# Kernel optimization log

Hardware: AMD Instinct MI355X
Metric: run time of the kernel (lower is better)

The kernel has to match this reference:

```python
import jax, jax.numpy as jnp
import numpy as np

B, C, H, W = 8, 256, 128, 128
CQ = C // 8


def setup_inputs() -> dict:
    key = jax.random.key(0)
    ks = jax.random.split(key, 8)
    s = 1.0 / np.sqrt(C)
    return {
        "x": jax.random.normal(ks[0], (B, C, H, W), dtype=jnp.float32),
        "wq": jax.random.normal(ks[1], (CQ, C), dtype=jnp.float32) * s,
        "bq": jax.random.normal(ks[2], (CQ,), dtype=jnp.float32) * 0.01,
        "wk": jax.random.normal(ks[3], (CQ, C), dtype=jnp.float32) * s,
        "bk": jax.random.normal(ks[4], (CQ,), dtype=jnp.float32) * 0.01,
        "wv": jax.random.normal(ks[5], (C, C), dtype=jnp.float32) * s,
        "bv": jax.random.normal(ks[6], (C,), dtype=jnp.float32) * 0.01,
        "gamma": jax.random.normal(ks[7], (1,), dtype=jnp.float32) * 0.1,
    }


def reference(x, wq, bq, wk, bk, wv, bv, gamma):
    b, c, h, w = x.shape
    # 1x1 convs == channel matmuls
    q = jnp.einsum("oc,bchw->bohw", wq, x) + bq[None, :, None, None]  # [B,Cq,H,W]
    k = jnp.einsum("oc,bchw->bohw", wk, x) + bk[None, :, None, None]  # [B,Cq,H,W]
    v = jnp.einsum("oc,bchw->bohw", wv, x) + bv[None, :, None, None]  # [B,C,H,W]

    # column (height) scores: energy_H[b,i,w,j] = <k[:, i, w], q[:, j, w]>, -inf on i==j
    e_h = jnp.einsum("bciw,bcjw->biwj", k, q)  # [B,H,W,H]
    diag = jnp.eye(h, dtype=bool)[:, None, :]  # [H,1,H] -> masks i==j
    e_h = jnp.where(diag[None], -jnp.inf, e_h)

    # row (width) scores: energy_W[b,h,i,j] = <k[:, h, i], q[:, h, j]>
    e_w = jnp.einsum("bchi,bchj->bhij", k, q)  # [B,H,W,W]

    # joint softmax over concatenated H+W scores (axis 3), as in the torch code
    att = jax.nn.softmax(jnp.concatenate([e_h, e_w], axis=3), axis=3)
    a_h, a_w = att[..., :h], att[..., h:]

    out_h = jnp.einsum("bciw,biwj->bcjw", v, a_h)  # aggregate along column
    out_w = jnp.einsum("bchi,bhij->bchj", v, a_w)  # aggregate along row
    return gamma * (out_h + out_w) + x
```

## Files before the change

### kernel.cpp

```cpp
#include <hip/hip_runtime.h>
#include <math.h>

#define C_   256
#define CQ_  32
#define H_   128
#define W_   128
#define HW_  (H_ * W_)
#define OC_  320

typedef __attribute__((ext_vector_type(8))) short  s8v;
typedef __attribute__((ext_vector_type(4))) float  f4v;
typedef __attribute__((ext_vector_type(8))) unsigned short u8v;
typedef __attribute__((ext_vector_type(4))) unsigned short u4v;

__device__ inline unsigned short f2bf(float f) {
    unsigned int u = __float_as_uint(f);
    unsigned int r = (u + 0x7fffu + ((u >> 16) & 1u)) >> 16;
    return (unsigned short)r;
}
__device__ inline float bfu(unsigned short u) {
    return __uint_as_float((unsigned int)u << 16);
}

__global__ __launch_bounds__(256) void k_wconv(
    const float* __restrict__ wq, const float* __restrict__ wk,
    const float* __restrict__ wv, unsigned short* __restrict__ Wb)
{
    int idx4 = blockIdx.x * 256 + threadIdx.x;
    int e = idx4 * 4;
    int oc = e >> 8, k = e & 255;
    const float* src;
    if (oc < 32)      src = wq + (size_t)oc * C_ + k;
    else if (oc < 64) src = wk + (size_t)(oc - 32) * C_ + k;
    else              src = wv + (size_t)(oc - 64) * C_ + k;
    float4 v = *(const float4*)src;
    u4v o;
    o[0] = f2bf(v.x); o[1] = f2bf(v.y); o[2] = f2bf(v.z); o[3] = f2bf(v.w);
    *(u4v*)(Wb + e) = o;
}

__global__ __launch_bounds__(256) void k_qkv(
    const float* __restrict__ x, const unsigned short* __restrict__ Wb,
    const float* __restrict__ bq, const float* __restrict__ bk,
    const float* __restrict__ bv,
    unsigned short* __restrict__ qkv, int b0)
{
    __shared__ __align__(16) unsigned short Wl[2][64][72];
    __shared__ __align__(16) unsigned int   Xp[2][32 * 132];
    const int t = threadIdx.x;
    const int lane = t & 63;
    const int wave = t >> 6;
    const int n0 = blockIdx.x * 128;
    const int ocblk = blockIdx.y * 64;
    const int bb = blockIdx.z;
    const float* xb = x + (size_t)(b0 + bb) * C_ * HW_;

    const int lg = lane >> 4;
    const int ll = lane & 15;
    const int n_w = wave * 32;

    const int kp8 = t >> 5;
    const int n4  = (t & 31) * 4;
    const int wrow = t >> 3;
    const int wcg  = (t & 7) * 8;
    float4 ra[4], rb[4];
    u8v wreg[2];

    #pragma unroll
    for (int p = 0; p < 4; ++p) {
        int krow = (p * 8 + kp8) * 2;
        ra[p] = *(const float4*)(xb + (size_t)krow * HW_ + n0 + n4);
        rb[p] = *(const float4*)(xb + (size_t)(krow + 1) * HW_ + n0 + n4);
    }
    #pragma unroll
    for (int q = 0; q < 2; ++q)
        wreg[q] = *(const u8v*)(Wb + (size_t)(ocblk + wrow + q * 32) * C_ + wcg);

    #pragma unroll
    for (int p = 0; p < 4; ++p) {
        uint4 d;
        const float* af  = (const float*)&ra[p];
        const float* bf_ = (const float*)&rb[p];
        #pragma unroll
        for (int i = 0; i < 4; ++i) {
            unsigned int lo = (__float_as_uint(af[i])  + 0x8000u) >> 16;
            unsigned int hi = (__float_as_uint(bf_[i]) + 0x8000u) & 0xffff0000u;
            ((unsigned int*)&d)[i] = hi | lo;
        }
        *(uint4*)&Xp[0][(p * 8 + kp8) * 132 + n4] = d;
    }
    #pragma unroll
    for (int q = 0; q < 2; ++q)
        *(u8v*)&Wl[0][wrow + q * 32][wcg] = wreg[q];

    #pragma unroll
    for (int p = 0; p < 4; ++p) {
        int krow = 64 + (p * 8 + kp8) * 2;
        ra[p] = *(const float4*)(xb + (size_t)krow * HW_ + n0 + n4);
        rb[p] = *(const float4*)(xb + (size_t)(krow + 1) * HW_ + n0 + n4);
    }
    #pragma unroll
    for (int q = 0; q < 2; ++q)
        wreg[q] = *(const u8v*)(Wb + (size_t)(ocblk + wrow + q * 32) * C_ + 64 + wcg);

    f4v acc[4][2];
    #pragma unroll
    for (int mr = 0; mr < 4; ++mr)
        #pragma unroll
        for (int nr = 0; nr < 2; ++nr)
            acc[mr][nr] = (f4v){0.f, 0.f, 0.f, 0.f};

    __syncthreads();

    #pragma unroll
    for (int kc = 0; kc < 4; ++kc) {
        const int cur = kc & 1;
        if (kc < 3) {
            #pragma unroll
            for (int p = 0; p < 4; ++p) {
                uint4 d;
                const float* af  = (const float*)&ra[p];
                const float* bf_ = (const float*)&rb[p];
                #pragma unroll
                for (int i = 0; i < 4; ++i) {
                    unsigned int lo = (__float_as_uint(af[i])  + 0x8000u) >> 16;
                    unsigned int hi = (__float_as_uint(bf_[i]) + 0x8000u) & 0xffff0000u;
                    ((unsigned int*)&d)[i] = hi | lo;
                }
                *(uint4*)&Xp[cur ^ 1][(p * 8 + kp8) * 132 + n4] = d;
            }
            #pragma unroll
            for (int q = 0; q < 2; ++q)
                *(u8v*)&Wl[cur ^ 1][wrow + q * 32][wcg] = wreg[q];
        }
        if (kc < 2) {
            #pragma unroll
            for (int p = 0; p < 4; ++p) {
                int krow = (kc + 2) * 64 + (p * 8 + kp8) * 2;
                ra[p] = *(const float4*)(xb + (size_t)krow * HW_ + n0 + n4);
                rb[p] = *(const float4*)(xb + (size_t)(krow + 1) * HW_ + n0 + n4);
            }
            #pragma unroll
            for (int q = 0; q < 2; ++q)
                wreg[q] = *(const u8v*)(
                    Wb + (size_t)(ocblk + wrow + q * 32) * C_ + (kc + 2) * 64 + wcg);
        }
        #pragma unroll
        for (int ks = 0; ks < 2; ++ks) {
            s8v afr[4];
            #pragma unroll
            for (int mr = 0; mr < 4; ++mr)
                afr[mr] = *(const s8v*)&Wl[cur][mr * 16 + ll][ks * 32 + lg * 8];
            #pragma unroll
            for (int nr = 0; nr < 2; ++nr) {
                int4 bd;
                #pragma unroll
                for (int e2 = 0; e2 < 4; ++e2)
                    ((int*)&bd)[e2] =
                        Xp[cur][(ks * 16 + lg * 4 + e2) * 132 + n_w + nr * 16 + ll];
                s8v bfr = *(s8v*)&bd;
                #pragma unroll
                for (int mr = 0; mr < 4; ++mr)
                    acc[mr][nr] = __builtin_amdgcn_mfma_f32_16x16x32_bf16(
                        afr[mr], bfr, acc[mr][nr], 0, 0, 0);
            }
        }
        __syncthreads();
    }

    #pragma unroll
    for (int mr = 0; mr < 4; ++mr) {
        float bias[4];
        #pragma unroll
        for (int r = 0; r < 4; ++r) {
            int oc = ocblk + mr * 16 + lg * 4 + r;
            if (oc < 32)      bias[r] = bq[oc];
            else if (oc < 64) bias[r] = bk[oc - 32];
            else              bias[r] = bv[oc - 64];
        }
        #pragma unroll
        for (int nr = 0; nr < 2; ++nr) {
            int n = n0 + n_w + nr * 16 + ll;
            #pragma unroll
            for (int r = 0; r < 4; ++r) {
                int oc = ocblk + mr * 16 + lg * 4 + r;
                qkv[((size_t)bb * OC_ + oc) * HW_ + n] = f2bf(acc[mr][nr][r] + bias[r]);
            }
        }
    }
}

__global__ __launch_bounds__(256) void k_transpose_qkv(
    const unsigned short* __restrict__ qkv, unsigned short* __restrict__ qkv_t)
{
    __shared__ unsigned short tile[32][34];
    const int bb = blockIdx.z;
    const int oc = blockIdx.y;
    const int th = (blockIdx.x & 3) * 32;
    const int tw = (blockIdx.x >> 2) * 32;
    const unsigned short* src = qkv + ((size_t)bb * OC_ + oc) * HW_;
    #pragma unroll
    for (int r = 0; r < 4; ++r) {
        int h = threadIdx.y * 4 + r;
        tile[h][threadIdx.x] = src[(size_t)(th + h) * W_ + tw + threadIdx.x];
    }
    __syncthreads();
    unsigned short* dst = qkv_t + (size_t)bb * W_ * OC_ * H_;
    #pragma unroll
    for (int r = 0; r < 4; ++r) {
        int wl = threadIdx.y * 4 + r;
        dst[((size_t)(tw + wl) * OC_ + oc) * H_ + th + threadIdx.x] = tile[threadIdx.x][wl];
    }
}

__device__ inline void stage_KQ(const unsigned short* base, int cstride,
                                unsigned int* Ktp, unsigned int* Qp, int t)
{
    {
        int i = t & 127, half = t >> 7, c0 = half * 16;
        unsigned int kr[16];
        #pragma unroll
        for (int cc = 0; cc < 16; ++cc)
            kr[cc] = base[(size_t)(32 + c0 + cc) * cstride + i];
        uint4 d0, d1;
        #pragma unroll
        for (int e2 = 0; e2 < 4; ++e2)
            ((unsigned int*)&d0)[e2] = kr[2 * e2] | (kr[2 * e2 + 1] << 16);
        #pragma unroll
        for (int e2 = 0; e2 < 4; ++e2)
            ((unsigned int*)&d1)[e2] = kr[8 + 2 * e2] | (kr[9 + 2 * e2] << 16);
        *(uint4*)&Ktp[i * 20 + half * 8]     = d0;
        *(uint4*)&Ktp[i * 20 + half * 8 + 4] = d1;
    }
    {
        int c2 = t >> 4, j8 = (t & 15) * 8;
        u8v qa = *(const u8v*)(base + (size_t)(2 * c2) * cstride + j8);
        u8v qb = *(const u8v*)(base + (size_t)(2 * c2 + 1) * cstride + j8);
        uint4 e0, e1;
        #pragma unroll
        for (int e = 0; e < 4; ++e)
            ((unsigned int*)&e0)[e] =
                (unsigned int)qa[e] | ((unsigned int)qb[e] << 16);
        #pragma unroll
        for (int e = 0; e < 4; ++e)
            ((unsigned int*)&e1)[e] =
                (unsigned int)qa[4 + e] | ((unsigned int)qb[4 + e] << 16);
        *(uint4*)&Qp[c2 * 132 + j8]     = e0;
        *(uint4*)&Qp[c2 * 132 + j8 + 4] = e1;
    }
}

__device__ inline f4v eqk_mfma(const unsigned int* Ktp, const unsigned int* Qp,
                               int mr, int j, int lg, int ll)
{
    s8v afr = *(const s8v*)&Ktp[(mr * 16 + ll) * 20 + lg * 4];
    int4 bd;
    #pragma unroll
    for (int e2 = 0; e2 < 4; ++e2)
        ((int*)&bd)[e2] = Qp[(lg * 4 + e2) * 132 + j];
    s8v bfr = *(s8v*)&bd;
    return __builtin_amdgcn_mfma_f32_16x16x32_bf16(
        afr, bfr, (f4v){0.f, 0.f, 0.f, 0.f}, 0, 0, 0);
}

__global__ __launch_bounds__(256) void k_stats_h(
    const unsigned short* __restrict__ qkv_t,
    float* __restrict__ mh, float* __restrict__ sh)
{
    __shared__ __align__(16) unsigned int Ktp[128 * 20];
    __shared__ __align__(16) unsigned int Qp[16 * 132];
    const int t = threadIdx.x;
    const int beta = blockIdx.x;
    const int bb = blockIdx.y;
    const unsigned short* base = qkv_t + ((size_t)bb * W_ + beta) * OC_ * H_;
    stage_KQ(base, H_, Ktp, Qp, t);
    __syncthreads();

    const int lane = t & 63;
    const int wv = t >> 6;
    const int lg = lane >> 4;
    const int ll = lane & 15;

    #pragma unroll
    for (int ml = 0; ml < 2; ++ml) {
        const int mr = wv * 2 + ml;
        const int i0 = mr * 16 + lg * 4;
        f4v ef[8];
        #pragma unroll
        for (int nt = 0; nt < 8; ++nt) {
            f4v e = eqk_mfma(Ktp, Qp, mr, nt * 16 + ll, lg, ll);
            int j = nt * 16 + ll;
            #pragma unroll
            for (int r = 0; r < 4; ++r)
                if (i0 + r == j) e[r] = -INFINITY;
            ef[nt] = e;
        }
        #pragma unroll
        for (int r = 0; r < 4; ++r) {
            float mm = -INFINITY;
            #pragma unroll
            for (int nt = 0; nt < 8; ++nt) mm = fmaxf(mm, ef[nt][r]);
            #pragma unroll
            for (int s = 1; s < 16; s <<= 1) mm = fmaxf(mm, __shfl_xor(mm, s));
            float ss = 0.f;
            #pragma unroll
            for (int nt = 0; nt < 8; ++nt) ss += __expf(ef[nt][r] - mm);
            #pragma unroll
            for (int s = 1; s < 16; s <<= 1) ss += __shfl_xor(ss, s);
            if (ll == 0) {
                int i = i0 + r;
                mh[((size_t)bb * H_ + i) * W_ + beta] = mm;
                sh[((size_t)bb * H_ + i) * W_ + beta] = ss;
            }
        }
    }
}

__global__ __launch_bounds__(256) void k_stats_w(
    const unsigned short* __restrict__ qkv,
    float* __restrict__ mw, float* __restrict__ sw)
{
    __shared__ __align__(16) unsigned int Ktp[128 * 20];
    __shared__ __align__(16) unsigned int Qp[16 * 132];
    const int t = threadIdx.x;
    const int alpha = blockIdx.x;
    const int bb = blockIdx.y;
    const unsigned short* base = qkv + (size_t)bb * OC_ * HW_ + (size_t)alpha * W_;
    stage_KQ(base, HW_, Ktp, Qp, t);
    __syncthreads();

    const int lane = t & 63;
    const int wv = t >> 6;
    const int lg = lane >> 4;
    const int ll = lane & 15;

    #pragma unroll
    for (int ml = 0; ml < 2; ++ml) {
        const int mr = wv * 2 + ml;
        const int i0 = mr * 16 + lg * 4;
        f4v ef[8];
        #pragma unroll
        for (int nt = 0; nt < 8; ++nt)
            ef[nt] = eqk_mfma(Ktp, Qp, mr, nt * 16 + ll, lg, ll);
        #pragma unroll
        for (int r = 0; r < 4; ++r) {
            float mm = -INFINITY;
            #pragma unroll
            for (int nt = 0; nt < 8; ++nt) mm = fmaxf(mm, ef[nt][r]);
            #pragma unroll
            for (int s = 1; s < 16; s <<= 1) mm = fmaxf(mm, __shfl_xor(mm, s));
            float ss = 0.f;
            #pragma unroll
            for (int nt = 0; nt < 8; ++nt) ss += __expf(ef[nt][r] - mm);
            #pragma unroll
            for (int s = 1; s < 16; s <<= 1) ss += __shfl_xor(ss, s);
            if (ll == 0) {
                int i = i0 + r;
                mw[((size_t)bb * H_ + alpha) * W_ + i] = mm;
                sw[((size_t)bb * H_ + alpha) * W_ + i] = ss;
            }
        }
    }
}

__global__ __launch_bounds__(256) void k_prep(
    const float* __restrict__ mh, const float* __restrict__ sh,
    const float* __restrict__ mw, const float* __restrict__ sw,
    float* __restrict__ mc, float* __restrict__ dv,
    float* __restrict__ mct, float* __restrict__ dvt, int n)
{
    int idx = blockIdx.x * 256 + threadIdx.x;
    if (idx >= n) return;
    float m1 = mh[idx], s1 = sh[idx], m2 = mw[idx], s2 = sw[idx];
    float m = fmaxf(m1, m2);
    float d = 1.f / (s1 * __expf(m1 - m) + s2 * __expf(m2 - m));
    mc[idx] = m; dv[idx] = d;
    int q = idx & (W_ - 1);
    int p = (idx >> 7) & (H_ - 1);
    int b = idx >> 14;
    size_t tid = ((size_t)b * W_ + q) * H_ + p;
    mct[tid] = m; dvt[tid] = d;
}

__global__ __launch_bounds__(256) void k_outh(
    const unsigned short* __restrict__ qkv_t,
    const float* __restrict__ mct, const float* __restrict__ dvt,
    unsigned short* __restrict__ oh_t)
{
    __shared__ __align__(16) unsigned short Pt[128 * 128];
    __shared__ __align__(16) unsigned char  Ubuf[18688];
    __shared__ float mloc[128], dloc[128];
    unsigned int* Ktp = (unsigned int*)Ubuf;
    unsigned int* Qp  = (unsigned int*)(Ubuf + 10240);
    unsigned short* Vl = (unsigned short*)Ubuf;

    const int t = threadIdx.x;
    const int beta = blockIdx.x;
    const int bb = blockIdx.y;
    const unsigned short* base = qkv_t + ((size_t)bb * W_ + beta) * OC_ * H_;

    if (t < 128) {
        size_t sidx = ((size_t)bb * W_ + beta) * H_ + t;
        mloc[t] = mct[sidx];
        dloc[t] = dvt[sidx];
    }
    stage_KQ(base, H_, Ktp, Qp, t);

    const int vc  = t >> 4;
    const int vi0 = (t & 15) * 8;
    u8v vreg[4];
    {
        const unsigned short* vsrc = base + (size_t)64 * H_;
        #pragma unroll
        for (int q = 0; q < 4; ++q)
            vreg[q] = *(const u8v*)(vsrc + (size_t)(vc + q * 16) * H_ + vi0);
    }
    __syncthreads();

    const int lane = t & 63;
    const int wv = t >> 6;
    const int lg = lane >> 4;
    const int ll = lane & 15;
    const int jq0 = wv * 32;

    #pragma unroll
    for (int mr = 0; mr < 8; ++mr) {
        const int i0 = mr * 16 + lg * 4;
        float mi[4], di[4];
        #pragma unroll
        for (int r = 0; r < 4; ++r) { mi[r] = mloc[i0 + r]; di[r] = dloc[i0 + r]; }
        #pragma unroll
        for (int nt = 0; nt < 2; ++nt) {
            int j = jq0 + nt * 16 + ll;
            f4v e = eqk_mfma(Ktp, Qp, mr, j, lg, ll);
            float p0 = (i0     == j) ? 0.f : __expf(e[0] - mi[0]) * di[0];
            float p1 = (i0 + 1 == j) ? 0.f : __expf(e[1] - mi[1]) * di[1];
            float p2 = (i0 + 2 == j) ? 0.f : __expf(e[2] - mi[2]) * di[2];
            float p3 = (i0 + 3 == j) ? 0.f : __expf(e[3] - mi[3]) * di[3];
            uint2 wd;
            wd.x = f2bf(p0) | ((unsigned int)f2bf(p1) << 16);
            wd.y = f2bf(p2) | ((unsigned int)f2bf(p3) << 16);
            int sidx = (j * 128 + i0) ^ ((j & 7) << 3);
            *(uint2*)&Pt[sidx] = wd;
        }
    }

    unsigned short* outbase = oh_t + ((size_t)bb * W_ + beta) * C_ * H_;
    const int cw = (wv & 1) * 32;
    const int jw = (wv >> 1) * 64;

    for (int ch = 0; ch < 4; ++ch) {
        __syncthreads();
        #pragma unroll
        for (int q = 0; q < 4; ++q) {
            int c = vc + q * 16;
            *(u8v*)&Vl[(c * 128 + vi0) ^ ((c & 7) << 3)] = vreg[q];
        }
        __syncthreads();
        if (ch < 3) {
            const unsigned short* vsrc = base + (size_t)(64 + (ch + 1) * 64) * H_;
            #pragma unroll
            for (int q = 0; q < 4; ++q)
                vreg[q] = *(const u8v*)(vsrc + (size_t)(vc + q * 16) * H_ + vi0);
        }

        f4v acc[2][4];
        #pragma unroll
        for (int cr = 0; cr < 2; ++cr)
            #pragma unroll
            for (int nt = 0; nt < 4; ++nt)
                acc[cr][nt] = (f4v){0.f, 0.f, 0.f, 0.f};

        #pragma unroll
        for (int kk = 0; kk < 4; ++kk) {
            s8v afr[2];
            #pragma unroll
            for (int cr = 0; cr < 2; ++cr) {
                int crow = cw + cr * 16 + ll;
                afr[cr] = *(const s8v*)&Vl[(crow * 128 + kk * 32 + lg * 8) ^ ((crow & 7) << 3)];
            }
            #pragma unroll
            for (int nt = 0; nt < 4; ++nt) {
                int j = jw + nt * 16 + ll;
                s8v bfr = *(const s8v*)&Pt[(j * 128 + kk * 32 + lg * 8) ^ ((j & 7) << 3)];
                acc[0][nt] = __builtin_amdgcn_mfma_f32_16x16x32_bf16(afr[0], bfr, acc[0][nt], 0, 0, 0);
                acc[1][nt] = __builtin_amdgcn_mfma_f32_16x16x32_bf16(afr[1], bfr, acc[1][nt], 0, 0, 0);
            }
        }
        #pragma unroll
        for (int cr = 0; cr < 2; ++cr)
            #pragma unroll
            for (int nt = 0; nt < 4; ++nt) {
                int j = jw + nt * 16 + ll;
                #pragma unroll
                for (int r = 0; r < 4; ++r) {
                    int c = ch * 64 + cw + cr * 16 + lg * 4 + r;
                    outbase[(size_t)c * H_ + j] = f2bf(acc[cr][nt][r]);
                }
            }
    }
}

__global__ __launch_bounds__(256) void k_outw(
    const unsigned short* __restrict__ qkv,
    const float* __restrict__ mc, const float* __restrict__ dv_,
    unsigned short* __restrict__ ow)
{
    __shared__ __align__(16) unsigned short Pt[128 * 128];
    __shared__ __align__(16) unsigned char  Ubuf[18688];
    __shared__ float mloc[128], dloc[128];
    unsigned int* Ktp = (unsigned int*)Ubuf;
    unsigned int* Qp  = (unsigned int*)(Ubuf + 10240);
    unsigned short* Vl = (unsigned short*)Ubuf;

    const int t = threadIdx.x;
    const int alpha = blockIdx.x;
    const int bb = blockIdx.y;
    const unsigned short* base = qkv + (size_t)bb * OC_ * HW_ + (size_t)alpha * W_;

    if (t < 128) {
        size_t sidx = ((size_t)bb * H_ + alpha) * W_ + t;
        mloc[t] = mc[sidx];
        dloc[t] = dv_[sidx];
    }
    stage_KQ(base, HW_, Ktp, Qp, t);

    const int vc  = t >> 4;
    const int vi0 = (t & 15) * 8;
    u8v vreg[4];
    {
        const unsigned short* vsrc = base + (size_t)64 * HW_;
        #pragma unroll
        for (int q = 0; q < 4; ++q)
            vreg[q] = *(const u8v*)(vsrc + (size_t)(vc + q * 16) * HW_ + vi0);
    }
    __syncthreads();

    const int lane = t & 63;
    const int wv = t >> 6;
    const int lg = lane >> 4;
    const int ll = lane & 15;
    const int jq0 = wv * 32;

    #pragma unroll
    for (int mr = 0; mr < 8; ++mr) {
        const int i0 = mr * 16 + lg * 4;
        float mi[4], di[4];
        #pragma unroll
        for (int r = 0; r < 4; ++r) { mi[r] = mloc[i0 + r]; di[r] = dloc[i0 + r]; }
        #pragma unroll
        for (int nt = 0; nt < 2; ++nt) {
            int j = jq0 + nt * 16 + ll;
            f4v e = eqk_mfma(Ktp, Qp, mr, j, lg, ll);
            float p0 = __expf(e[0] - mi[0]) * di[0];
            float p1 = __expf(e[1] - mi[1]) * di[1];
            float p2 = __expf(e[2] - mi[2]) * di[2];
            float p3 = __expf(e[3] - mi[3]) * di[3];
            uint2 wd;
            wd.x = f2bf(p0) | ((unsigned int)f2bf(p1) << 16);
            wd.y = f2bf(p2) | ((unsigned int)f2bf(p3) << 16);
            int sidx = (j * 128 + i0) ^ ((j & 7) << 3);
            *(uint2*)&Pt[sidx] = wd;
        }
    }

    unsigned short* obase = ow + (size_t)bb * C_ * HW_ + (size_t)alpha * W_;
    const int cw = (wv & 1) * 32;
    const int jw = (wv >> 1) * 64;

    for (int ch = 0; ch < 4; ++ch) {
        __syncthreads();
        #pragma unroll
        for (int q = 0; q < 4; ++q) {
            int c = vc + q * 16;
            *(u8v*)&Vl[(c * 128 + vi0) ^ ((c & 7) << 3)] = vreg[q];
        }
        __syncthreads();
        if (ch < 3) {
            const unsigned short* vsrc = base + (size_t)(64 + (ch + 1) * 64) * HW_;
            #pragma unroll
            for (int q = 0; q < 4; ++q)
                vreg[q] = *(const u8v*)(vsrc + (size_t)(vc + q * 16) * HW_ + vi0);
        }

        f4v acc[2][4];
        #pragma unroll
        for (int cr = 0; cr < 2; ++cr)
            #pragma unroll
            for (int nt = 0; nt < 4; ++nt)
                acc[cr][nt] = (f4v){0.f, 0.f, 0.f, 0.f};

        #pragma unroll
        for (int kk = 0; kk < 4; ++kk) {
            s8v afr[2];
            #pragma unroll
            for (int cr = 0; cr < 2; ++cr) {
                int crow = cw + cr * 16 + ll;
                afr[cr] = *(const s8v*)&Vl[(crow * 128 + kk * 32 + lg * 8) ^ ((crow & 7) << 3)];
            }
            #pragma unroll
            for (int nt = 0; nt < 4; ++nt) {
                int j = jw + nt * 16 + ll;
                s8v bfr = *(const s8v*)&Pt[(j * 128 + kk * 32 + lg * 8) ^ ((j & 7) << 3)];
                acc[0][nt] = __builtin_amdgcn_mfma_f32_16x16x32_bf16(afr[0], bfr, acc[0][nt], 0, 0, 0);
                acc[1][nt] = __builtin_amdgcn_mfma_f32_16x16x32_bf16(afr[1], bfr, acc[1][nt], 0, 0, 0);
            }
        }
        #pragma unroll
        for (int cr = 0; cr < 2; ++cr)
            #pragma unroll
            for (int nt = 0; nt < 4; ++nt) {
                int j = jw + nt * 16 + ll;
                #pragma unroll
                for (int r = 0; r < 4; ++r) {
                    int c = ch * 64 + cw + cr * 16 + lg * 4 + r;
                    obase[(size_t)c * HW_ + j] = f2bf(acc[cr][nt][r]);
                }
            }
    }
}

__global__ __launch_bounds__(256) void k_combine(
    const unsigned short* __restrict__ oh_t, const unsigned short* __restrict__ ow,
    const float* __restrict__ x, const float* __restrict__ gamma_p,
    float* __restrict__ out, int b0)
{
    __shared__ unsigned short tile[128][130];
    const int t  = threadIdx.x;
    const int c  = blockIdx.x;
    const int bb = blockIdx.y;
    const float gamma = gamma_p[0];

    {
        const unsigned short* src = oh_t + (size_t)bb * W_ * C_ * H_ + (size_t)c * H_;
        const int row = t >> 1;
        const int h0  = (t & 1) * 64;
        #pragma unroll
        for (int q = 0; q < 8; ++q) {
            u8v v = *(const u8v*)(src + (size_t)row * (C_ * H_) + h0 + q * 8);
            *(u8v*)&tile[row][h0 + q * 8] = v;
        }
    }
    __syncthreads();

    const size_t pbase = ((size_t)bb * C_ + c) * HW_;
    const size_t gbase = ((size_t)(b0 + bb) * C_ + c) * HW_;
    const int w4 = (t & 31) * 4;
    const int hb = t >> 5;
    #pragma unroll
    for (int hh = 0; hh < 16; ++hh) {
        int h = hb + hh * 8;
        size_t idx = (size_t)h * W_ + w4;
        float4 xv = *(const float4*)(x + gbase + idx);
        u4v o4 = *(const u4v*)(ow + pbase + idx);
        float4 r;
        r.x = xv.x + gamma * (bfu(o4[0]) + bfu(tile[w4 + 0][h]));
        r.y = xv.y + gamma * (bfu(o4[1]) + bfu(tile[w4 + 1][h]));
        r.z = xv.z + gamma * (bfu(o4[2]) + bfu(tile[w4 + 2][h]));
        r.w = xv.w + gamma * (bfu(o4[3]) + bfu(tile[w4 + 3][h]));
        *(float4*)(out + gbase + idx) = r;
    }
}

extern "C" void kernel_launch(void* const* d_in, const int* in_sizes, int n_in,
                              void* d_out, int out_size, void* d_ws, size_t ws_size,
                              hipStream_t stream)
{
    (void)in_sizes; (void)n_in; (void)out_size;
    const float* x  = (const float*)d_in[0];
    const float* wq = (const float*)d_in[1];
    const float* bq = (const float*)d_in[2];
    const float* wk = (const float*)d_in[3];
    const float* bk = (const float*)d_in[4];
    const float* wv = (const float*)d_in[5];
    const float* bv = (const float*)d_in[6];
    const float* gm = (const float*)d_in[7];
    float* out = (float*)d_out;

    const size_t e_qkv  = (size_t)OC_ * HW_;
    const size_t e_out  = (size_t)C_ * HW_;
    const size_t e_stat = (size_t)HW_;
    const size_t perb_bytes = (e_qkv * 2 + e_out * 2) * 2 + e_stat * 8 * 4;
    const size_t wb_bytes = (size_t)OC_ * C_ * 2;
    int nbcap = (int)((ws_size - wb_bytes) / perb_bytes);
    if (nbcap > 8) nbcap = 8;
    if (nbcap < 1) nbcap = 1;

    unsigned short* Wb    = (unsigned short*)d_ws;
    unsigned short* qkv   = Wb    + (size_t)OC_ * C_;
    unsigned short* qkv_t = qkv   + e_qkv * nbcap;
    unsigned short* oh    = qkv_t + e_qkv * nbcap;
    unsigned short* ow    = oh    + e_out * nbcap;
    float* mh  = (float*)(ow + e_out * nbcap);
    float* sh  = mh  + e_stat * nbcap;
    float* mw  = sh  + e_stat * nbcap;
    float* sw  = mw  + e_stat * nbcap;
    float* mc  = sw  + e_stat * nbcap;
    float* dv  = mc  + e_stat * nbcap;
    float* mct = dv  + e_stat * nbcap;
    float* dvt = mct + e_stat * nbcap;

    k_wconv<<<dim3(80), 256, 0, stream>>>(wq, wk, wv, Wb);

    for (int b0 = 0; b0 < 8; b0 += nbcap) {
        int nb = 8 - b0 < nbcap ? 8 - b0 : nbcap;
        k_qkv<<<dim3(HW_ / 128, 5, nb), 256, 0, stream>>>(
            x, Wb, bq, bk, bv, qkv, b0);
        k_transpose_qkv<<<dim3(16, OC_, nb), dim3(32, 8), 0, stream>>>(qkv, qkv_t);
        k_stats_h<<<dim3(W_, nb), 256, 0, stream>>>(qkv_t, mh, sh);
        k_stats_w<<<dim3(H_, nb), 256, 0, stream>>>(qkv, mw, sw);
        int nstat = nb * HW_;
        k_prep<<<dim3((nstat + 255) / 256), 256, 0, stream>>>(
            mh, sh, mw, sw, mc, dv, mct, dvt, nstat);
        k_outh<<<dim3(W_, nb), 256, 0, stream>>>(qkv_t, mct, dvt, oh);
        k_outw<<<dim3(H_, nb), 256, 0, stream>>>(qkv, mc, dv, ow);
        k_combine<<<dim3(C_, nb), 256, 0, stream>>>(
            oh, ow, x, gm, out, b0);
    }
}
```

Before: 289.6 us.

## Merge stats kernels, raise MFMA wave priority, use nontemporal loads in combine

Merges the height and width softmax-statistics kernels into one launch, picking the mode from a grid dimension. This removes a launch and lets both halves fill the GPU together. It also wraps the MFMA loops in the qkv and output kernels with s_setprio to favour matrix-core waves. The combine kernel switches to nontemporal loads and stores for its streaming data. The priority hints and cache bypass may help or hurt depending on how waves interleave and how the data is reused.

```diff
diff --git a/kernel.cpp b/kernel.cpp
--- a/kernel.cpp
+++ b/kernel.cpp
@@ -145,6 +145,7 @@
                 wreg[q] = *(const u8v*)(
                     Wb + (size_t)(ocblk + wrow + q * 32) * C_ + (kc + 2) * 64 + wcg);
         }
+        __builtin_amdgcn_s_setprio(1);
         #pragma unroll
         for (int ks = 0; ks < 2; ++ks) {
             s8v afr[4];
@@ -165,6 +166,7 @@
                         afr[mr], bfr, acc[mr][nr], 0, 0, 0);
             }
         }
+        __builtin_amdgcn_s_setprio(0);
         __syncthreads();
     }
 
@@ -263,17 +265,27 @@
         afr, bfr, (f4v){0.f, 0.f, 0.f, 0.f}, 0, 0, 0);
 }
 
-__global__ __launch_bounds__(256) void k_stats_h(
-    const unsigned short* __restrict__ qkv_t,
-    float* __restrict__ mh, float* __restrict__ sh)
+__global__ __launch_bounds__(256) void k_stats(
+    const unsigned short* __restrict__ qkv_t, const unsigned short* __restrict__ qkv,
+    float* __restrict__ mh, float* __restrict__ sh,
+    float* __restrict__ mw, float* __restrict__ sw)
 {
     __shared__ __align__(16) unsigned int Ktp[128 * 20];
     __shared__ __align__(16) unsigned int Qp[16 * 132];
     const int t = threadIdx.x;
-    const int beta = blockIdx.x;
-    const int bb = blockIdx.y;
-    const unsigned short* base = qkv_t + ((size_t)bb * W_ + beta) * OC_ * H_;
-    stage_KQ(base, H_, Ktp, Qp, t);
+    const int pos = blockIdx.x;
+    const int mode = blockIdx.y;
+    const int bb = blockIdx.z;
+    const unsigned short* base;
+    int cstride;
+    if (mode == 0) {
+        base = qkv_t + ((size_t)bb * W_ + pos) * OC_ * H_;
+        cstride = H_;
+    } else {
+        base = qkv + (size_t)bb * OC_ * HW_ + (size_t)pos * W_;
+        cstride = HW_;
+    }
+    stage_KQ(base, cstride, Ktp, Qp, t);
     __syncthreads();
 
     const int lane = t & 63;
@@ -289,10 +301,12 @@
         #pragma unroll
         for (int nt = 0; nt < 8; ++nt) {
             f4v e = eqk_mfma(Ktp, Qp, mr, nt * 16 + ll, lg, ll);
-            int j = nt * 16 + ll;
-            #pragma unroll
-            for (int r = 0; r < 4; ++r)
-                if (i0 + r == j) e[r] = -INFINITY;
+            if (mode == 0) {
+                int j = nt * 16 + ll;
+                #pragma unroll
+                for (int r = 0; r < 4; ++r)
+                    if (i0 + r == j) e[r] = -INFINITY;
+            }
             ef[nt] = e;
         }
         #pragma unroll
@@ -309,55 +323,13 @@
             for (int s = 1; s < 16; s <<= 1) ss += __shfl_xor(ss, s);
             if (ll == 0) {
                 int i = i0 + r;
-                mh[((size_t)bb * H_ + i) * W_ + beta] = mm;
-                sh[((size_t)bb * H_ + i) * W_ + beta] = ss;
-            }
-        }
-    }
-}
-
-__global__ __launch_bounds__(256) void k_stats_w(
-    const unsigned short* __restrict__ qkv,
-    float* __restrict__ mw, float* __restrict__ sw)
-{
-    __shared__ __align__(16) unsigned int Ktp[128 * 20];
-    __shared__ __align__(16) unsigned int Qp[16 * 132];
-    const int t = threadIdx.x;
-    const int alpha = blockIdx.x;
-    const int bb = blockIdx.y;
-    const unsigned short* base = qkv + (size_t)bb * OC_ * HW_ + (size_t)alpha * W_;
-    stage_KQ(base, HW_, Ktp, Qp, t);
-    __syncthreads();
-
-    const int lane = t & 63;
-    const int wv = t >> 6;
-    const int lg = lane >> 4;
-    const int ll = lane & 15;
-
-    #pragma unroll
-    for (int ml = 0; ml < 2; ++ml) {
-        const int mr = wv * 2 + ml;
-        const int i0 = mr * 16 + lg * 4;
-        f4v ef[8];
-        #pragma unroll
-        for (int nt = 0; nt < 8; ++nt)
-            ef[nt] = eqk_mfma(Ktp, Qp, mr, nt * 16 + ll, lg, ll);
-        #pragma unroll
-        for (int r = 0; r < 4; ++r) {
-            float mm = -INFINITY;
-            #pragma unroll
-            for (int nt = 0; nt < 8; ++nt) mm = fmaxf(mm, ef[nt][r]);
-            #pragma unroll
-            for (int s = 1; s < 16; s <<= 1) mm = fmaxf(mm, __shfl_xor(mm, s));
-            float ss = 0.f;
-            #pragma unroll
-            for (int nt = 0; nt < 8; ++nt) ss += __expf(ef[nt][r] - mm);
-            #pragma unroll
-            for (int s = 1; s < 16; s <<= 1) ss += __shfl_xor(ss, s);
-            if (ll == 0) {
-                int i = i0 + r;
-                mw[((size_t)bb * H_ + alpha) * W_ + i] = mm;
-                sw[((size_t)bb * H_ + alpha) * W_ + i] = ss;
+                if (mode == 0) {
+                    mh[((size_t)bb * H_ + i) * W_ + pos] = mm;
+                    sh[((size_t)bb * H_ + i) * W_ + pos] = ss;
+                } else {
+                    mw[((size_t)bb * H_ + pos) * W_ + i] = mm;
+                    sw[((size_t)bb * H_ + pos) * W_ + i] = ss;
+                }
             }
         }
     }
@@ -423,6 +395,7 @@
     const int ll = lane & 15;
     const int jq0 = wv * 32;
 
+    __builtin_amdgcn_s_setprio(1);
     #pragma unroll
     for (int mr = 0; mr < 8; ++mr) {
         const int i0 = mr * 16 + lg * 4;
@@ -444,6 +417,7 @@
             *(uint2*)&Pt[sidx] = wd;
         }
     }
+    __builtin_amdgcn_s_setprio(0);
 
     unsigned short* outbase = oh_t + ((size_t)bb * W_ + beta) * C_ * H_;
     const int cw = (wv & 1) * 32;
@@ -471,6 +445,7 @@
             for (int nt = 0; nt < 4; ++nt)
                 acc[cr][nt] = (f4v){0.f, 0.f, 0.f, 0.f};
 
+        __builtin_amdgcn_s_setprio(1);
         #pragma unroll
         for (int kk = 0; kk < 4; ++kk) {
             s8v afr[2];
@@ -487,6 +462,7 @@
                 acc[1][nt] = __builtin_amdgcn_mfma_f32_16x16x32_bf16(afr[1], bfr, acc[1][nt], 0, 0, 0);
             }
         }
+        __builtin_amdgcn_s_setprio(0);
         #pragma unroll
         for (int cr = 0; cr < 2; ++cr)
             #pragma unroll
@@ -542,6 +518,7 @@
     const int ll = lane & 15;
     const int jq0 = wv * 32;
 
+    __builtin_amdgcn_s_setprio(1);
     #pragma unroll
     for (int mr = 0; mr < 8; ++mr) {
         const int i0 = mr * 16 + lg * 4;
@@ -563,6 +540,7 @@
             *(uint2*)&Pt[sidx] = wd;
         }
     }
+    __builtin_amdgcn_s_setprio(0);
 
     unsigned short* obase = ow + (size_t)bb * C_ * HW_ + (size_t)alpha * W_;
     const int cw = (wv & 1) * 32;
@@ -590,6 +568,7 @@
             for (int nt = 0; nt < 4; ++nt)
                 acc[cr][nt] = (f4v){0.f, 0.f, 0.f, 0.f};
 
+        __builtin_amdgcn_s_setprio(1);
         #pragma unroll
         for (int kk = 0; kk < 4; ++kk) {
             s8v afr[2];
@@ -606,6 +585,7 @@
                 acc[1][nt] = __builtin_amdgcn_mfma_f32_16x16x32_bf16(afr[1], bfr, acc[1][nt], 0, 0, 0);
             }
         }
+        __builtin_amdgcn_s_setprio(0);
         #pragma unroll
         for (int cr = 0; cr < 2; ++cr)
             #pragma unroll
@@ -637,7 +617,8 @@
         const int h0  = (t & 1) * 64;
         #pragma unroll
         for (int q = 0; q < 8; ++q) {
-            u8v v = *(const u8v*)(src + (size_t)row * (C_ * H_) + h0 + q * 8);
+            u8v v = __builtin_nontemporal_load(
+                (const u8v*)(src + (size_t)row * (C_ * H_) + h0 + q * 8));
             *(u8v*)&tile[row][h0 + q * 8] = v;
         }
     }
@@ -651,14 +632,14 @@
     for (int hh = 0; hh < 16; ++hh) {
         int h = hb + hh * 8;
         size_t idx = (size_t)h * W_ + w4;
-        float4 xv = *(const float4*)(x + gbase + idx);
-        u4v o4 = *(const u4v*)(ow + pbase + idx);
-        float4 r;
-        r.x = xv.x + gamma * (bfu(o4[0]) + bfu(tile[w4 + 0][h]));
-        r.y = xv.y + gamma * (bfu(o4[1]) + bfu(tile[w4 + 1][h]));
-        r.z = xv.z + gamma * (bfu(o4[2]) + bfu(tile[w4 + 2][h]));
-        r.w = xv.w + gamma * (bfu(o4[3]) + bfu(tile[w4 + 3][h]));
-        *(float4*)(out + gbase + idx) = r;
+        f4v xv = __builtin_nontemporal_load((const f4v*)(x + gbase + idx));
+        u4v o4 = __builtin_nontemporal_load((const u4v*)(ow + pbase + idx));
+        f4v r;
+        r[0] = xv[0] + gamma * (bfu(o4[0]) + bfu(tile[w4 + 0][h]));
+        r[1] = xv[1] + gamma * (bfu(o4[1]) + bfu(tile[w4 + 1][h]));
+        r[2] = xv[2] + gamma * (bfu(o4[2]) + bfu(tile[w4 + 2][h]));
+        r[3] = xv[3] + gamma * (bfu(o4[3]) + bfu(tile[w4 + 3][h]));
+        __builtin_nontemporal_store(r, (f4v*)(out + gbase + idx));
     }
 }
 
@@ -707,8 +688,8 @@
         k_qkv<<<dim3(HW_ / 128, 5, nb), 256, 0, stream>>>(
             x, Wb, bq, bk, bv, qkv, b0);
         k_transpose_qkv<<<dim3(16, OC_, nb), dim3(32, 8), 0, stream>>>(qkv, qkv_t);
-        k_stats_h<<<dim3(W_, nb), 256, 0, stream>>>(qkv_t, mh, sh);
-        k_stats_w<<<dim3(H_, nb), 256, 0, stream>>>(qkv, mw, sw);
+        k_stats<<<dim3(128, 2, nb), 256, 0, stream>>>(
+            qkv_t, qkv, mh, sh, mw, sw);
         int nstat = nb * HW_;
         k_prep<<<dim3((nstat + 255) / 256), 256, 0, stream>>>(
             mh, sh, mw, sw, mc, dv, mct, dvt, nstat);
```

Result: no change. 290.1 us (+0.2%).
